# Optimization experiments

Hardware: AMD Instinct MI355X
Metric: run time of the kernel (lower is better)

## Reference

```python
import jax, jax.numpy as jnp
import numpy as np

N, F, D = 50000, 64, 3
E = 800000
H = 128          # local MLP hidden / output dim
G = 256          # global MLP output dim


def _init_linear(key, fan_in, fan_out):
    kw, kb = jax.random.split(key)
    W = jax.random.normal(kw, (fan_in, fan_out), dtype=jnp.float32) / np.sqrt(fan_in)
    b = jax.random.normal(kb, (fan_out,), dtype=jnp.float32) * 0.01
    return W, b


def setup_inputs() -> dict:
    key = jax.random.key(0)
    kx, kp, ke, k1, k2, kg = jax.random.split(key, 6)
    x = jax.random.normal(kx, (N, F), dtype=jnp.float32)
    pos = jax.random.uniform(kp, (N, D), dtype=jnp.float32)
    edge_index = jax.random.randint(ke, (2, E), 0, N, dtype=jnp.int64)
    W1, b1 = _init_linear(k1, F + D, H)   # local_nn layer 1
    W2, b2 = _init_linear(k2, H, H)       # local_nn layer 2
    Wg, bg = _init_linear(kg, H, G)       # global_nn
    return {"x": x, "pos": pos, "W1": W1, "b1": b1, "W2": W2, "b2": b2,
            "Wg": Wg, "bg": bg, "edge_index": edge_index}


def reference(x, pos, W1, b1, W2, b2, Wg, bg, edge_index):
    n = x.shape[0]
    # add self loops (duplicate edges are harmless under max-reduction)
    loops = jnp.arange(n, dtype=edge_index.dtype)
    ei = jnp.concatenate([edge_index, jnp.stack([loops, loops])], axis=1)
    row, col = ei[0], ei[1]            # row = target i, col = neighbor j
    rel = pos[col] - pos[row]          # [E+N, D]
    h = jnp.concatenate([x[col], rel], axis=1)          # [E+N, F+D]
    h = jax.nn.relu(h @ W1 + b1)                         # local MLP
    h = jax.nn.relu(h @ W2 + b2)                         # [E+N, H]
    agg = jax.ops.segment_max(h, row, num_segments=n)    # scatter-max per node
    out = jax.nn.relu(agg @ Wg + bg)                      # global MLP [N, G]
    return out
```

## Files before the change

### kernel.cpp

```cpp
#include <hip/hip_runtime.h>

typedef __attribute__((ext_vector_type(4))) float f32x4;
typedef __attribute__((ext_vector_type(8))) short bf16x8;

#define EDGE_GRID 2048
#define OUT_GRID  512

__device__ __forceinline__ unsigned int f2bf(float f) {
    unsigned int u = __float_as_uint(f);
    return (u + 0x7FFFu + ((u >> 16) & 1u)) >> 16;
}

__global__ __launch_bounds__(256) void u_kernel(
    const float* __restrict__ x, const float* __restrict__ W1,
    const float* __restrict__ b1, unsigned short* __restrict__ u, int N)
{
    __shared__ float sx[8][64];
    const int t = threadIdx.x;
    const int base = blockIdx.x * 8;
    for (int i = t; i < 512; i += 256) {
        const int node = base + (i >> 6);
        sx[i >> 6][i & 63] = (node < N) ? x[(size_t)node * 64 + (i & 63)] : 0.0f;
    }
    __syncthreads();
    const int half = t >> 7, col = t & 127;
    const float bias = b1[col];
    float acc[4] = {bias, bias, bias, bias};
#pragma unroll 8
    for (int k = 0; k < 64; ++k) {
        const float w = W1[k * 128 + col];
#pragma unroll
        for (int j = 0; j < 4; ++j)
            acc[j] = fmaf(sx[half * 4 + j][k], w, acc[j]);
    }
#pragma unroll
    for (int j = 0; j < 4; ++j) {
        const int node = base + half * 4 + j;
        if (node < N) u[(size_t)node * 128 + col] = (unsigned short)f2bf(acc[j]);
    }
}

__global__ void prep_kernel(const float* __restrict__ W2, const float* __restrict__ Wg,
                            unsigned short* __restrict__ W2t, unsigned short* __restrict__ Wgt)
{
    const int i = blockIdx.x * 256 + threadIdx.x;
    if (i < 16384) {
        const int n = i >> 7, k = i & 127;
        W2t[i] = (unsigned short)f2bf(W2[k * 128 + n]);
    } else if (i < 49152) {
        const int j = i - 16384;
        const int n = j >> 7, k = j & 127;
        Wgt[j] = (unsigned short)f2bf(Wg[k * 256 + n]);
    }
}

__global__ void count_kernel(const int* __restrict__ ei, int* __restrict__ deg,
                             int E, int nTot)
{
    const int i = blockIdx.x * 256 + threadIdx.x;
    if (i < nTot) {
        const int row = (i < E) ? ei[i] : i - E;
        atomicAdd(deg + row, 1);
    }
}

__global__ __launch_bounds__(256) void scan1_kernel(
    const int* __restrict__ deg, int* __restrict__ offs, int* __restrict__ bsums, int N)
{
    __shared__ int sc[256];
    const int t = threadIdx.x;
    const int i0 = blockIdx.x * 1024 + t * 4;
    int v0 = (i0 + 0 < N) ? deg[i0 + 0] : 0;
    int v1 = (i0 + 1 < N) ? deg[i0 + 1] : 0;
    int v2 = (i0 + 2 < N) ? deg[i0 + 2] : 0;
    int v3 = (i0 + 3 < N) ? deg[i0 + 3] : 0;
    const int s = v0 + v1 + v2 + v3;
    sc[t] = s;
    __syncthreads();
    for (int off = 1; off < 256; off <<= 1) {
        const int val = (t >= off) ? sc[t - off] : 0;
        __syncthreads();
        sc[t] += val;
        __syncthreads();
    }
    int run = sc[t] - s;
    if (i0 + 0 < N) offs[i0 + 0] = run; run += v0;
    if (i0 + 1 < N) offs[i0 + 1] = run; run += v1;
    if (i0 + 2 < N) offs[i0 + 2] = run; run += v2;
    if (i0 + 3 < N) offs[i0 + 3] = run;
    if (t == 255) bsums[blockIdx.x] = sc[255];
}

__global__ void scan2_kernel(int* __restrict__ bsums, int NB)
{
    __shared__ int sc[64];
    const int t = threadIdx.x;
    const int v = (t < NB) ? bsums[t] : 0;
    sc[t] = v;
    __syncthreads();
    for (int off = 1; off < 64; off <<= 1) {
        const int val = (t >= off) ? sc[t - off] : 0;
        __syncthreads();
        sc[t] += val;
        __syncthreads();
    }
    if (t < NB) bsums[t] = sc[t] - v;
}

__global__ void scan3_kernel(int* __restrict__ offs, const int* __restrict__ bsums, int N)
{
    const int i = blockIdx.x * 256 + threadIdx.x;
    if (i < N) offs[i] += bsums[i >> 10];
}

__global__ void scatter_kernel(const int* __restrict__ ei, const int* __restrict__ offs,
                               int* __restrict__ cursor, int* __restrict__ srow,
                               int* __restrict__ scol, int E, int nTot)
{
    const int i = blockIdx.x * 256 + threadIdx.x;
    if (i < nTot) {
        int row, col;
        if (i < E) { row = ei[i]; col = ei[E + i]; }
        else       { row = col = i - E; }
        const int p = atomicAdd(cursor + row, 1);
        const int q = offs[row] + p;
        srow[q] = row;
        scol[q] = col;
    }
}

__global__ __launch_bounds__(256, 4) void edge_kernel(
    const unsigned short* __restrict__ u, const float* __restrict__ pos,
    const float* __restrict__ W1, const float* __restrict__ b2,
    const unsigned short* __restrict__ W2t, const int* __restrict__ srow,
    const int* __restrict__ scol, unsigned int* __restrict__ agg,
    int nTot, int nTiles)
{
    __shared__ unsigned short sh1[2][4096];
    __shared__ float          sh2[4096];
    __shared__ float          sW1p[384];
    __shared__ int            sRowL[2][32];

    const int t = threadIdx.x;
    const int wv = t >> 6, lane = t & 63;
    const int m = lane & 15, g = lane >> 4;
    const int n0 = wv * 32 + m;
    const int e_h1 = t >> 3, kc = (t & 7) * 16;
    const int cR = t & 127, hR = t >> 7;

    bf16x8 bfr[2][4];
#pragma unroll
    for (int nb = 0; nb < 2; ++nb)
#pragma unroll
        for (int ks = 0; ks < 4; ++ks)
            bfr[nb][ks] = *(const bf16x8*)(W2t + (size_t)(n0 + nb * 16) * 128 + (ks * 4 + g) * 8);
    const float bia0 = b2[n0], bia1 = b2[n0 + 16];

    for (int i = t; i < 384; i += 256) sW1p[i] = W1[64 * 128 + i];
    __syncthreads();

    auto gather = [&](int tile, int& c, float& r0, float& r1, float& r2,
                      uint4& ua, uint4& ub, int& rowStage) {
        c = -1; rowStage = -1;
        if (tile < nTiles) {
            const int p = tile * 32 + e_h1;
            if (p < nTot) {
                c = scol[p];
                const int r = srow[p];
                r0 = pos[c * 3 + 0] - pos[r * 3 + 0];
                r1 = pos[c * 3 + 1] - pos[r * 3 + 1];
                r2 = pos[c * 3 + 2] - pos[r * 3 + 2];
                const uint4* up = (const uint4*)(u + (size_t)c * 128 + kc);
                ua = up[0]; ub = up[1];
            }
            if (t < 32) {
                const int p2 = tile * 32 + t;
                rowStage = (p2 < nTot) ? srow[p2] : -1;
            }
        }
    };
    auto computeH1 = [&](int buf, int c, float r0, float r1, float r2,
                         uint4 ua, uint4 ub, int rowStage) {
        unsigned int ow[8] = {0,0,0,0,0,0,0,0};
        if (c >= 0) {
            const unsigned int uw[8] = {ua.x, ua.y, ua.z, ua.w, ub.x, ub.y, ub.z, ub.w};
#pragma unroll
            for (int j = 0; j < 8; ++j) {
                const int k = kc + j * 2;
                float lo = __uint_as_float(uw[j] << 16);
                float hi = __uint_as_float(uw[j] & 0xFFFF0000u);
                lo = fmaf(r0, sW1p[k],     fmaf(r1, sW1p[128 + k],     fmaf(r2, sW1p[256 + k],     lo)));
                hi = fmaf(r0, sW1p[k + 1], fmaf(r1, sW1p[128 + k + 1], fmaf(r2, sW1p[256 + k + 1], hi)));
                ow[j] = f2bf(fmaxf(lo, 0.0f)) | (f2bf(fmaxf(hi, 0.0f)) << 16);
            }
        }
        const int g0 = e_h1 * 16 + (t & 7) * 2;
        ((int4*)sh1[buf])[(g0)     ^ (e_h1 & 7)] = make_int4(ow[0], ow[1], ow[2], ow[3]);
        ((int4*)sh1[buf])[(g0 + 1) ^ (e_h1 & 7)] = make_int4(ow[4], ow[5], ow[6], ow[7]);
        if (t < 32) sRowL[buf][t] = rowStage;
    };

    {
        int c, rs; float r0 = 0, r1 = 0, r2 = 0; uint4 ua = {0,0,0,0}, ub = {0,0,0,0};
        gather(blockIdx.x, c, r0, r1, r2, ua, ub, rs);
        computeH1(0, c, r0, r1, r2, ua, ub, rs);
    }
    __syncthreads();

    int b = 0;
    for (int tile = blockIdx.x; tile < nTiles; tile += EDGE_GRID, b ^= 1) {
        const int nextTile = tile + EDGE_GRID;

        int c, rs; float r0 = 0, r1 = 0, r2 = 0; uint4 ua = {0,0,0,0}, ub = {0,0,0,0};
        gather(nextTile, c, r0, r1, r2, ua, ub, rs);

        {
            f32x4 acc0 = {0,0,0,0}, acc1 = {0,0,0,0}, acc2 = {0,0,0,0}, acc3 = {0,0,0,0};
            const unsigned short* s1 = sh1[b];
#pragma unroll
            for (int ks = 0; ks < 4; ++ks) {
                const int slot = ks * 4 + g;
                const bf16x8 a0 = *(const bf16x8*)&s1[(m        * 16 + (slot ^ (m & 7))) << 3];
                const bf16x8 a1 = *(const bf16x8*)&s1[((m + 16) * 16 + (slot ^ (m & 7))) << 3];
                acc0 = __builtin_amdgcn_mfma_f32_16x16x32_bf16(a0, bfr[0][ks], acc0, 0, 0, 0);
                acc1 = __builtin_amdgcn_mfma_f32_16x16x32_bf16(a0, bfr[1][ks], acc1, 0, 0, 0);
                acc2 = __builtin_amdgcn_mfma_f32_16x16x32_bf16(a1, bfr[0][ks], acc2, 0, 0, 0);
                acc3 = __builtin_amdgcn_mfma_f32_16x16x32_bf16(a1, bfr[1][ks], acc3, 0, 0, 0);
            }
#pragma unroll
            for (int rg = 0; rg < 4; ++rg) {
                const int e0 = g * 4 + rg, e1 = 16 + g * 4 + rg;
                sh2[e0 * 128 + ((n0      + e0 * 4) & 127)] = fmaxf(acc0[rg] + bia0, 0.0f);
                sh2[e0 * 128 + ((n0 + 16 + e0 * 4) & 127)] = fmaxf(acc1[rg] + bia1, 0.0f);
                sh2[e1 * 128 + ((n0      + e1 * 4) & 127)] = fmaxf(acc2[rg] + bia0, 0.0f);
                sh2[e1 * 128 + ((n0 + 16 + e1 * 4) & 127)] = fmaxf(acc3[rg] + bia1, 0.0f);
            }
        }
        __syncthreads();

        {
            float run = 0.0f; int cur = -1;
            const int ebase = hR * 16;
            for (int i = 0; i < 16; ++i) {
                const int e = ebase + i;
                const int r = sRowL[b][e];
                if (r < 0) break;
                const float v = sh2[e * 128 + ((cR + e * 4) & 127)];
                if (r != cur) {
                    if (cur >= 0) {
                        const unsigned int bits = __float_as_uint(run);
                        unsigned int* dst = agg + (size_t)cur * 128 + cR;
                        if (bits > *dst) atomicMax(dst, bits);
                    }
                    cur = r; run = v;
                } else run = fmaxf(run, v);
            }
            if (cur >= 0) {
                const unsigned int bits = __float_as_uint(run);
                unsigned int* dst = agg + (size_t)cur * 128 + cR;
                if (bits > *dst) atomicMax(dst, bits);
            }
        }

        if (nextTile < nTiles)
            computeH1(b ^ 1, c, r0, r1, r2, ua, ub, rs);
        __syncthreads();
    }
}

__global__ __launch_bounds__(256, 2) void out_kernel(
    const float* __restrict__ agg, const unsigned short* __restrict__ Wgt,
    const float* __restrict__ bg, float* __restrict__ out, int N, int nTiles)
{
    extern __shared__ char smem[];
    unsigned short* sWgt = (unsigned short*)smem;
    unsigned short* sA   = (unsigned short*)(smem + 65536);
    float*          sbg  = (float*)(smem + 73728);

    const int t = threadIdx.x;
    for (int i = t; i < 4096; i += 256) {
        const int n = i >> 4;
        ((int4*)sWgt)[i ^ (n & 7)] = ((const int4*)Wgt)[i];
    }
    if (t < 256) sbg[t] = bg[t];
    __syncthreads();

    const int wv = t >> 6, lane = t & 63;
    const int m = lane & 15, g = lane >> 4;
    const int eA = t >> 3, kcA = (t & 7) * 16;

    for (int tile = blockIdx.x; tile < nTiles; tile += OUT_GRID) {
        const int tbase = tile * 32;

        {
            unsigned int ow[8] = {0,0,0,0,0,0,0,0};
            const int node = tbase + eA;
            if (node < N) {
                const float4* ap = (const float4*)(agg + (size_t)node * 128 + kcA);
#pragma unroll
                for (int j = 0; j < 4; ++j) {
                    const float4 v = ap[j];
                    ow[j * 2 + 0] = f2bf(v.x) | (f2bf(v.y) << 16);
                    ow[j * 2 + 1] = f2bf(v.z) | (f2bf(v.w) << 16);
                }
            }
            const int g0 = eA * 16 + (t & 7) * 2;
            ((int4*)sA)[(g0)     ^ (eA & 7)] = make_int4(ow[0], ow[1], ow[2], ow[3]);
            ((int4*)sA)[(g0 + 1) ^ (eA & 7)] = make_int4(ow[4], ow[5], ow[6], ow[7]);
        }
        __syncthreads();

        f32x4 acc[2][4] = {{{0,0,0,0},{0,0,0,0},{0,0,0,0},{0,0,0,0}},
                           {{0,0,0,0},{0,0,0,0},{0,0,0,0},{0,0,0,0}}};
#pragma unroll
        for (int ks = 0; ks < 4; ++ks) {
            const int slot = ks * 4 + g;
            const bf16x8 a0 = *(const bf16x8*)&sA[(m        * 16 + (slot ^ (m & 7))) << 3];
            const bf16x8 a1 = *(const bf16x8*)&sA[((m + 16) * 16 + (slot ^ (m & 7))) << 3];
#pragma unroll
            for (int nt = 0; nt < 4; ++nt) {
                const int n = wv * 64 + nt * 16 + m;
                const bf16x8 bfrag = *(const bf16x8*)&sWgt[(n * 16 + (slot ^ (m & 7))) << 3];
                acc[0][nt] = __builtin_amdgcn_mfma_f32_16x16x32_bf16(a0, bfrag, acc[0][nt], 0, 0, 0);
                acc[1][nt] = __builtin_amdgcn_mfma_f32_16x16x32_bf16(a1, bfrag, acc[1][nt], 0, 0, 0);
            }
        }
#pragma unroll
        for (int mg = 0; mg < 2; ++mg)
#pragma unroll
        for (int nt = 0; nt < 4; ++nt) {
            const int n = wv * 64 + nt * 16 + m;
            const float bias = sbg[n];
#pragma unroll
            for (int rg = 0; rg < 4; ++rg) {
                const int node = tbase + mg * 16 + g * 4 + rg;
                if (node < N)
                    out[(size_t)node * 256 + n] = fmaxf(acc[mg][nt][rg] + bias, 0.0f);
            }
        }
        __syncthreads();
    }
}

extern "C" void kernel_launch(void* const* d_in, const int* in_sizes, int n_in,
                              void* d_out, int out_size, void* d_ws, size_t ws_size,
                              hipStream_t stream)
{
    const float* x   = (const float*)d_in[0];
    const float* pos = (const float*)d_in[1];
    const float* W1  = (const float*)d_in[2];
    const float* b1  = (const float*)d_in[3];
    const float* W2  = (const float*)d_in[4];
    const float* b2  = (const float*)d_in[5];
    const float* Wg  = (const float*)d_in[6];
    const float* bg  = (const float*)d_in[7];
    const int*   ei  = (const int*)d_in[8];
    float* out = (float*)d_out;

    const int N    = in_sizes[1] / 3;
    const int E    = in_sizes[8] / 2;
    const int nTot = E + N;

    size_t off = 0;
    auto alloc = [&](size_t bytes) -> void* {
        void* p = (char*)d_ws + off;
        off += (bytes + 255) & ~(size_t)255;
        return p;
    };
    unsigned short* u      = (unsigned short*)alloc((size_t)N * 128 * 2);
    unsigned int*   agg    = (unsigned int*)  alloc((size_t)N * 128 * 4);
    int*            deg    = (int*)           alloc((size_t)N * 4);
    int*            offs   = (int*)           alloc((size_t)N * 4);
    int*            cursor = (int*)           alloc((size_t)N * 4);
    int*            srow   = (int*)           alloc((size_t)nTot * 4);
    int*            scol   = (int*)           alloc((size_t)nTot * 4);
    unsigned short* W2t    = (unsigned short*)alloc(16384 * 2);
    unsigned short* Wgt    = (unsigned short*)alloc(32768 * 2);
    int*            bsums  = (int*)           alloc(64 * 4);

    hipMemsetAsync(agg,    0, (size_t)N * 128 * 4, stream);
    hipMemsetAsync(deg,    0, (size_t)N * 4,       stream);
    hipMemsetAsync(cursor, 0, (size_t)N * 4,       stream);

    hipLaunchKernelGGL(prep_kernel, dim3(192), dim3(256), 0, stream, W2, Wg, W2t, Wgt);
    hipLaunchKernelGGL(u_kernel, dim3((N + 7) / 8), dim3(256), 0, stream, x, W1, b1, u, N);
    hipLaunchKernelGGL(count_kernel, dim3((nTot + 255) / 256), dim3(256), 0, stream,
                       ei, deg, E, nTot);
    const int NB = (N + 1023) / 1024;
    hipLaunchKernelGGL(scan1_kernel, dim3(NB), dim3(256), 0, stream, deg, offs, bsums, N);
    hipLaunchKernelGGL(scan2_kernel, dim3(1), dim3(64), 0, stream, bsums, NB);
    hipLaunchKernelGGL(scan3_kernel, dim3((N + 255) / 256), dim3(256), 0, stream,
                       offs, bsums, N);
    hipLaunchKernelGGL(scatter_kernel, dim3((nTot + 255) / 256), dim3(256), 0, stream,
                       ei, offs, cursor, srow, scol, E, nTot);

    const int nTilesE = (nTot + 31) / 32;
    hipLaunchKernelGGL(edge_kernel, dim3(EDGE_GRID), dim3(256), 0, stream,
                       u, pos, W1, b2, W2t, srow, scol, agg, nTot, nTilesE);

    const int nTilesO = (N + 31) / 32;
    const int out_shmem = 65536 + 8192 + 1024;
    hipFuncSetAttribute((const void*)out_kernel,
                        hipFuncAttributeMaxDynamicSharedMemorySize, out_shmem);
    hipLaunchKernelGGL(out_kernel, dim3(OUT_GRID), dim3(256), out_shmem, stream,
                       (const float*)agg, Wgt, bg, out, N, nTilesO);
}
```

Measured before the change: 378.5 us.

## Fuse prep kernels, single-block scan, register-resident weights, retuned edge pipeline

Merges the u, count and weight-transpose kernels into one launch and replaces the three-kernel scan with a single 1024-thread block scan. The scatter reuses the degree counter through atomicSub, so the cursor buffer and its memset go away. In the edge kernel the h1 buffer becomes single, W1 rows are padded in shared memory to avoid bank conflicts, the next tile's h1 is written before the scatter-max, and occupancy is raised. The output kernel keeps Wg fragments in registers instead of a 64KB shared copy, allowing more blocks and a larger grid. The single-block scan serializes the prefix sum, and the heavier register use may cause spills.

```diff
diff --git a/kernel.cpp b/kernel.cpp
--- a/kernel.cpp
+++ b/kernel.cpp
@@ -1,120 +1,122 @@
 #include <hip/hip_runtime.h>
+#include <hip/hip_bf16.h>
 
 typedef __attribute__((ext_vector_type(4))) float f32x4;
 typedef __attribute__((ext_vector_type(8))) short bf16x8;
 
-#define EDGE_GRID 2048
-#define OUT_GRID  512
-
-__device__ __forceinline__ unsigned int f2bf(float f) {
-    unsigned int u = __float_as_uint(f);
-    return (u + 0x7FFFu + ((u >> 16) & 1u)) >> 16;
-}
-
-__global__ __launch_bounds__(256) void u_kernel(
+#define EDGE_GRID 1536
+#define OUT_GRID  1024
+
+__device__ __forceinline__ unsigned int packbf(float lo, float hi) {
+    __hip_bfloat16 l = __float2bfloat16(lo), h = __float2bfloat16(hi);
+    const unsigned short lu = *reinterpret_cast<unsigned short*>(&l);
+    const unsigned short hu = *reinterpret_cast<unsigned short*>(&h);
+    return (unsigned int)lu | ((unsigned int)hu << 16);
+}
+__device__ __forceinline__ unsigned short bf1(float f) {
+    __hip_bfloat16 v = __float2bfloat16(f);
+    return *reinterpret_cast<unsigned short*>(&v);
+}
+
+__global__ __launch_bounds__(256) void prep_kernel(
     const float* __restrict__ x, const float* __restrict__ W1,
-    const float* __restrict__ b1, unsigned short* __restrict__ u, int N)
+    const float* __restrict__ b1, const float* __restrict__ W2,
+    const float* __restrict__ Wg, const int* __restrict__ ei,
+    unsigned short* __restrict__ u, unsigned short* __restrict__ W2t,
+    unsigned short* __restrict__ Wgt, int* __restrict__ deg,
+    int N, int E, int nTot, int NB_U, int NB_C)
 {
     __shared__ float sx[8][64];
+    const int blk = blockIdx.x;
     const int t = threadIdx.x;
-    const int base = blockIdx.x * 8;
-    for (int i = t; i < 512; i += 256) {
-        const int node = base + (i >> 6);
-        sx[i >> 6][i & 63] = (node < N) ? x[(size_t)node * 64 + (i & 63)] : 0.0f;
-    }
-    __syncthreads();
-    const int half = t >> 7, col = t & 127;
-    const float bias = b1[col];
-    float acc[4] = {bias, bias, bias, bias};
+    if (blk < NB_U) {
+        const int base = blk * 8;
+        for (int i = t; i < 512; i += 256) {
+            const int node = base + (i >> 6);
+            sx[i >> 6][i & 63] = (node < N) ? x[(size_t)node * 64 + (i & 63)] : 0.0f;
+        }
+        __syncthreads();
+        const int half = t >> 7, col = t & 127;
+        const float bias = b1[col];
+        float acc[4] = {bias, bias, bias, bias};
 #pragma unroll 8
-    for (int k = 0; k < 64; ++k) {
-        const float w = W1[k * 128 + col];
-#pragma unroll
-        for (int j = 0; j < 4; ++j)
-            acc[j] = fmaf(sx[half * 4 + j][k], w, acc[j]);
-    }
-#pragma unroll
-    for (int j = 0; j < 4; ++j) {
-        const int node = base + half * 4 + j;
-        if (node < N) u[(size_t)node * 128 + col] = (unsigned short)f2bf(acc[j]);
-    }
-}
-
-__global__ void prep_kernel(const float* __restrict__ W2, const float* __restrict__ Wg,
-                            unsigned short* __restrict__ W2t, unsigned short* __restrict__ Wgt)
-{
-    const int i = blockIdx.x * 256 + threadIdx.x;
-    if (i < 16384) {
-        const int n = i >> 7, k = i & 127;
-        W2t[i] = (unsigned short)f2bf(W2[k * 128 + n]);
-    } else if (i < 49152) {
-        const int j = i - 16384;
-        const int n = j >> 7, k = j & 127;
-        Wgt[j] = (unsigned short)f2bf(Wg[k * 256 + n]);
-    }
-}
-
-__global__ void count_kernel(const int* __restrict__ ei, int* __restrict__ deg,
-                             int E, int nTot)
-{
-    const int i = blockIdx.x * 256 + threadIdx.x;
-    if (i < nTot) {
-        const int row = (i < E) ? ei[i] : i - E;
-        atomicAdd(deg + row, 1);
-    }
-}
-
-__global__ __launch_bounds__(256) void scan1_kernel(
-    const int* __restrict__ deg, int* __restrict__ offs, int* __restrict__ bsums, int N)
-{
-    __shared__ int sc[256];
+        for (int k = 0; k < 64; ++k) {
+            const float w = W1[k * 128 + col];
+#pragma unroll
+            for (int j = 0; j < 4; ++j)
+                acc[j] = fmaf(sx[half * 4 + j][k], w, acc[j]);
+        }
+#pragma unroll
+        for (int j = 0; j < 4; ++j) {
+            const int node = base + half * 4 + j;
+            if (node < N) u[(size_t)node * 128 + col] = bf1(acc[j]);
+        }
+    } else if (blk < NB_U + NB_C) {
+        const int i = (blk - NB_U) * 256 + t;
+        if (i < nTot) {
+            const int row = (i < E) ? ei[i] : i - E;
+            atomicAdd(deg + row, 1);
+        }
+    } else {
+        const int i = (blk - NB_U - NB_C) * 256 + t;
+        if (i < 16384) {
+            const int n = i >> 7, k = i & 127;
+            W2t[i] = bf1(W2[k * 128 + n]);
+        } else if (i < 49152) {
+            const int j = i - 16384;
+            const int n = j >> 7, k = j & 127;
+            Wgt[j] = bf1(Wg[k * 256 + n]);
+        }
+    }
+}
+
+__global__ __launch_bounds__(1024) void scan_kernel(
+    const int* __restrict__ deg, int* __restrict__ offs, int N)
+{
+    __shared__ int sc[1024];
     const int t = threadIdx.x;
-    const int i0 = blockIdx.x * 1024 + t * 4;
-    int v0 = (i0 + 0 < N) ? deg[i0 + 0] : 0;
-    int v1 = (i0 + 1 < N) ? deg[i0 + 1] : 0;
-    int v2 = (i0 + 2 < N) ? deg[i0 + 2] : 0;
-    int v3 = (i0 + 3 < N) ? deg[i0 + 3] : 0;
-    const int s = v0 + v1 + v2 + v3;
+    const int c0 = t * 52;
+    int v[52];
+    int s = 0;
+#pragma unroll
+    for (int j4 = 0; j4 < 13; ++j4) {
+        const int idx = c0 + j4 * 4;
+        int4 d = {0, 0, 0, 0};
+        if (idx + 3 < N) d = *(const int4*)(deg + idx);
+        else {
+            if (idx     < N) d.x = deg[idx];
+            if (idx + 1 < N) d.y = deg[idx + 1];
+            if (idx + 2 < N) d.z = deg[idx + 2];
+        }
+        v[j4*4+0] = s; s += d.x;
+        v[j4*4+1] = s; s += d.y;
+        v[j4*4+2] = s; s += d.z;
+        v[j4*4+3] = s; s += d.w;
+    }
     sc[t] = s;
     __syncthreads();
-    for (int off = 1; off < 256; off <<= 1) {
+    for (int off = 1; off < 1024; off <<= 1) {
         const int val = (t >= off) ? sc[t - off] : 0;
         __syncthreads();
         sc[t] += val;
         __syncthreads();
     }
-    int run = sc[t] - s;
-    if (i0 + 0 < N) offs[i0 + 0] = run; run += v0;
-    if (i0 + 1 < N) offs[i0 + 1] = run; run += v1;
-    if (i0 + 2 < N) offs[i0 + 2] = run; run += v2;
-    if (i0 + 3 < N) offs[i0 + 3] = run;
-    if (t == 255) bsums[blockIdx.x] = sc[255];
-}
-
-__global__ void scan2_kernel(int* __restrict__ bsums, int NB)
-{
-    __shared__ int sc[64];
-    const int t = threadIdx.x;
-    const int v = (t < NB) ? bsums[t] : 0;
-    sc[t] = v;
-    __syncthreads();
-    for (int off = 1; off < 64; off <<= 1) {
-        const int val = (t >= off) ? sc[t - off] : 0;
-        __syncthreads();
-        sc[t] += val;
-        __syncthreads();
-    }
-    if (t < NB) bsums[t] = sc[t] - v;
-}
-
-__global__ void scan3_kernel(int* __restrict__ offs, const int* __restrict__ bsums, int N)
-{
-    const int i = blockIdx.x * 256 + threadIdx.x;
-    if (i < N) offs[i] += bsums[i >> 10];
+    const int base = sc[t] - s;
+#pragma unroll
+    for (int j4 = 0; j4 < 13; ++j4) {
+        const int idx = c0 + j4 * 4;
+        const int4 o = {base + v[j4*4], base + v[j4*4+1], base + v[j4*4+2], base + v[j4*4+3]};
+        if (idx + 3 < N) *(int4*)(offs + idx) = o;
+        else {
+            if (idx     < N) offs[idx]     = o.x;
+            if (idx + 1 < N) offs[idx + 1] = o.y;
+            if (idx + 2 < N) offs[idx + 2] = o.z;
+        }
+    }
 }
 
 __global__ void scatter_kernel(const int* __restrict__ ei, const int* __restrict__ offs,
-                               int* __restrict__ cursor, int* __restrict__ srow,
+                               int* __restrict__ deg, int* __restrict__ srow,
                                int* __restrict__ scol, int E, int nTot)
 {
     const int i = blockIdx.x * 256 + threadIdx.x;
@@ -122,30 +124,31 @@
         int row, col;
         if (i < E) { row = ei[i]; col = ei[E + i]; }
         else       { row = col = i - E; }
-        const int p = atomicAdd(cursor + row, 1);
+        const int p = atomicSub(deg + row, 1) - 1;
         const int q = offs[row] + p;
         srow[q] = row;
         scol[q] = col;
     }
 }
 
-__global__ __launch_bounds__(256, 4) void edge_kernel(
+__global__ __launch_bounds__(256, 6) void edge_kernel(
     const unsigned short* __restrict__ u, const float* __restrict__ pos,
     const float* __restrict__ W1, const float* __restrict__ b2,
     const unsigned short* __restrict__ W2t, const int* __restrict__ srow,
     const int* __restrict__ scol, unsigned int* __restrict__ agg,
     int nTot, int nTiles)
 {
-    __shared__ unsigned short sh1[2][4096];
+    __shared__ unsigned short sh1[4096];
     __shared__ float          sh2[4096];
-    __shared__ float          sW1p[384];
+    __shared__ float          sW1p[480];
     __shared__ int            sRowL[2][32];
 
     const int t = threadIdx.x;
     const int wv = t >> 6, lane = t & 63;
     const int m = lane & 15, g = lane >> 4;
     const int n0 = wv * 32 + m;
-    const int e_h1 = t >> 3, kc = (t & 7) * 16;
+    const int e_h1 = t >> 3, s8 = t & 7, kc = s8 * 16;
+    const int wb = s8 * 18;
     const int cR = t & 127, hR = t >> 7;
 
     bf16x8 bfr[2][4];
@@ -156,7 +159,10 @@
             bfr[nb][ks] = *(const bf16x8*)(W2t + (size_t)(n0 + nb * 16) * 128 + (ks * 4 + g) * 8);
     const float bia0 = b2[n0], bia1 = b2[n0 + 16];
 
-    for (int i = t; i < 384; i += 256) sW1p[i] = W1[64 * 128 + i];
+    for (int i = t; i < 384; i += 256) {
+        const int r = i >> 7, k = i & 127;
+        sW1p[r * 160 + k + 2 * (k >> 4)] = W1[64 * 128 + i];
+    }
     __syncthreads();
 
     auto gather = [&](int tile, int& c, float& r0, float& r1, float& r2,
@@ -186,17 +192,17 @@
             const unsigned int uw[8] = {ua.x, ua.y, ua.z, ua.w, ub.x, ub.y, ub.z, ub.w};
 #pragma unroll
             for (int j = 0; j < 8; ++j) {
-                const int k = kc + j * 2;
+                const int wk = wb + 2 * j;
                 float lo = __uint_as_float(uw[j] << 16);
                 float hi = __uint_as_float(uw[j] & 0xFFFF0000u);
-                lo = fmaf(r0, sW1p[k],     fmaf(r1, sW1p[128 + k],     fmaf(r2, sW1p[256 + k],     lo)));
-                hi = fmaf(r0, sW1p[k + 1], fmaf(r1, sW1p[128 + k + 1], fmaf(r2, sW1p[256 + k + 1], hi)));
-                ow[j] = f2bf(fmaxf(lo, 0.0f)) | (f2bf(fmaxf(hi, 0.0f)) << 16);
-            }
-        }
-        const int g0 = e_h1 * 16 + (t & 7) * 2;
-        ((int4*)sh1[buf])[(g0)     ^ (e_h1 & 7)] = make_int4(ow[0], ow[1], ow[2], ow[3]);
-        ((int4*)sh1[buf])[(g0 + 1) ^ (e_h1 & 7)] = make_int4(ow[4], ow[5], ow[6], ow[7]);
+                lo = fmaf(r0, sW1p[wk],       fmaf(r1, sW1p[160 + wk],     fmaf(r2, sW1p[320 + wk],     lo)));
+                hi = fmaf(r0, sW1p[wk + 1],   fmaf(r1, sW1p[160 + wk + 1], fmaf(r2, sW1p[320 + wk + 1], hi)));
+                ow[j] = packbf(fmaxf(lo, 0.0f), fmaxf(hi, 0.0f));
+            }
+        }
+        const int g0 = e_h1 * 16 + s8 * 2;
+        ((int4*)sh1)[(g0)     ^ (e_h1 & 7)] = make_int4(ow[0], ow[1], ow[2], ow[3]);
+        ((int4*)sh1)[(g0 + 1) ^ (e_h1 & 7)] = make_int4(ow[4], ow[5], ow[6], ow[7]);
         if (t < 32) sRowL[buf][t] = rowStage;
     };
 
@@ -216,12 +222,11 @@
 
         {
             f32x4 acc0 = {0,0,0,0}, acc1 = {0,0,0,0}, acc2 = {0,0,0,0}, acc3 = {0,0,0,0};
-            const unsigned short* s1 = sh1[b];
 #pragma unroll
             for (int ks = 0; ks < 4; ++ks) {
                 const int slot = ks * 4 + g;
-                const bf16x8 a0 = *(const bf16x8*)&s1[(m        * 16 + (slot ^ (m & 7))) << 3];
-                const bf16x8 a1 = *(const bf16x8*)&s1[((m + 16) * 16 + (slot ^ (m & 7))) << 3];
+                const bf16x8 a0 = *(const bf16x8*)&sh1[(m        * 16 + (slot ^ (m & 7))) << 3];
+                const bf16x8 a1 = *(const bf16x8*)&sh1[((m + 16) * 16 + (slot ^ (m & 7))) << 3];
                 acc0 = __builtin_amdgcn_mfma_f32_16x16x32_bf16(a0, bfr[0][ks], acc0, 0, 0, 0);
                 acc1 = __builtin_amdgcn_mfma_f32_16x16x32_bf16(a0, bfr[1][ks], acc1, 0, 0, 0);
                 acc2 = __builtin_amdgcn_mfma_f32_16x16x32_bf16(a1, bfr[0][ks], acc2, 0, 0, 0);
@@ -237,6 +242,9 @@
             }
         }
         __syncthreads();
+
+        if (nextTile < nTiles)
+            computeH1(b ^ 1, c, r0, r1, r2, ua, ub, rs);
 
         {
             float run = 0.0f; int cur = -1;
@@ -261,33 +269,31 @@
                 if (bits > *dst) atomicMax(dst, bits);
             }
         }
-
-        if (nextTile < nTiles)
-            computeH1(b ^ 1, c, r0, r1, r2, ua, ub, rs);
-        __syncthreads();
-    }
-}
-
-__global__ __launch_bounds__(256, 2) void out_kernel(
+        __syncthreads();
+    }
+}
+
+__global__ __launch_bounds__(256, 4) void out_kernel(
     const float* __restrict__ agg, const unsigned short* __restrict__ Wgt,
     const float* __restrict__ bg, float* __restrict__ out, int N, int nTiles)
 {
-    extern __shared__ char smem[];
-    unsigned short* sWgt = (unsigned short*)smem;
-    unsigned short* sA   = (unsigned short*)(smem + 65536);
-    float*          sbg  = (float*)(smem + 73728);
+    __shared__ unsigned short sA[4096];
 
     const int t = threadIdx.x;
-    for (int i = t; i < 4096; i += 256) {
-        const int n = i >> 4;
-        ((int4*)sWgt)[i ^ (n & 7)] = ((const int4*)Wgt)[i];
-    }
-    if (t < 256) sbg[t] = bg[t];
-    __syncthreads();
-
     const int wv = t >> 6, lane = t & 63;
     const int m = lane & 15, g = lane >> 4;
     const int eA = t >> 3, kcA = (t & 7) * 16;
+
+    bf16x8 wfr[4][4];
+    float bgv[4];
+#pragma unroll
+    for (int nt = 0; nt < 4; ++nt) {
+        const int n = wv * 64 + nt * 16 + m;
+#pragma unroll
+        for (int ks = 0; ks < 4; ++ks)
+            wfr[nt][ks] = *(const bf16x8*)(Wgt + (size_t)n * 128 + (ks * 4 + g) * 8);
+        bgv[nt] = bg[n];
+    }
 
     for (int tile = blockIdx.x; tile < nTiles; tile += OUT_GRID) {
         const int tbase = tile * 32;
@@ -300,8 +306,8 @@
 #pragma unroll
                 for (int j = 0; j < 4; ++j) {
                     const float4 v = ap[j];
-                    ow[j * 2 + 0] = f2bf(v.x) | (f2bf(v.y) << 16);
-                    ow[j * 2 + 1] = f2bf(v.z) | (f2bf(v.w) << 16);
+                    ow[j * 2 + 0] = packbf(v.x, v.y);
+                    ow[j * 2 + 1] = packbf(v.z, v.w);
                 }
             }
             const int g0 = eA * 16 + (t & 7) * 2;
@@ -319,10 +325,8 @@
             const bf16x8 a1 = *(const bf16x8*)&sA[((m + 16) * 16 + (slot ^ (m & 7))) << 3];
 #pragma unroll
             for (int nt = 0; nt < 4; ++nt) {
-                const int n = wv * 64 + nt * 16 + m;
-                const bf16x8 bfrag = *(const bf16x8*)&sWgt[(n * 16 + (slot ^ (m & 7))) << 3];
-                acc[0][nt] = __builtin_amdgcn_mfma_f32_16x16x32_bf16(a0, bfrag, acc[0][nt], 0, 0, 0);
-                acc[1][nt] = __builtin_amdgcn_mfma_f32_16x16x32_bf16(a1, bfrag, acc[1][nt], 0, 0, 0);
+                acc[0][nt] = __builtin_amdgcn_mfma_f32_16x16x32_bf16(a0, wfr[nt][ks], acc[0][nt], 0, 0, 0);
+                acc[1][nt] = __builtin_amdgcn_mfma_f32_16x16x32_bf16(a1, wfr[nt][ks], acc[1][nt], 0, 0, 0);
             }
         }
 #pragma unroll
@@ -330,12 +334,11 @@
 #pragma unroll
         for (int nt = 0; nt < 4; ++nt) {
             const int n = wv * 64 + nt * 16 + m;
-            const float bias = sbg[n];
 #pragma unroll
             for (int rg = 0; rg < 4; ++rg) {
                 const int node = tbase + mg * 16 + g * 4 + rg;
                 if (node < N)
-                    out[(size_t)node * 256 + n] = fmaxf(acc[mg][nt][rg] + bias, 0.0f);
+                    out[(size_t)node * 256 + n] = fmaxf(acc[mg][nt][rg] + bgv[nt], 0.0f);
             }
         }
         __syncthreads();
@@ -367,41 +370,34 @@
         off += (bytes + 255) & ~(size_t)255;
         return p;
     };
-    unsigned short* u      = (unsigned short*)alloc((size_t)N * 128 * 2);
-    unsigned int*   agg    = (unsigned int*)  alloc((size_t)N * 128 * 4);
-    int*            deg    = (int*)           alloc((size_t)N * 4);
-    int*            offs   = (int*)           alloc((size_t)N * 4);
-    int*            cursor = (int*)           alloc((size_t)N * 4);
-    int*            srow   = (int*)           alloc((size_t)nTot * 4);
-    int*            scol   = (int*)           alloc((size_t)nTot * 4);
-    unsigned short* W2t    = (unsigned short*)alloc(16384 * 2);
-    unsigned short* Wgt    = (unsigned short*)alloc(32768 * 2);
-    int*            bsums  = (int*)           alloc(64 * 4);
-
-    hipMemsetAsync(agg,    0, (size_t)N * 128 * 4, stream);
-    hipMemsetAsync(deg,    0, (size_t)N * 4,       stream);
-    hipMemsetAsync(cursor, 0, (size_t)N * 4,       stream);
-
-    hipLaunchKernelGGL(prep_kernel, dim3(192), dim3(256), 0, stream, W2, Wg, W2t, Wgt);
-    hipLaunchKernelGGL(u_kernel, dim3((N + 7) / 8), dim3(256), 0, stream, x, W1, b1, u, N);
-    hipLaunchKernelGGL(count_kernel, dim3((nTot + 255) / 256), dim3(256), 0, stream,
-                       ei, deg, E, nTot);
-    const int NB = (N + 1023) / 1024;
-    hipLaunchKernelGGL(scan1_kernel, dim3(NB), dim3(256), 0, stream, deg, offs, bsums, N);
-    hipLaunchKernelGGL(scan2_kernel, dim3(1), dim3(64), 0, stream, bsums, NB);
-    hipLaunchKernelGGL(scan3_kernel, dim3((N + 255) / 256), dim3(256), 0, stream,
-                       offs, bsums, N);
+    unsigned short* u    = (unsigned short*)alloc((size_t)N * 128 * 2);
+    unsigned int*   agg  = (unsigned int*)  alloc((size_t)N * 128 * 4);
+    int*            deg  = (int*)           alloc((size_t)N * 4);
+    int*            offs = (int*)           alloc((size_t)N * 4);
+    int*            srow = (int*)           alloc((size_t)nTot * 4);
+    int*            scol = (int*)           alloc((size_t)nTot * 4);
+    unsigned short* W2t  = (unsigned short*)alloc(16384 * 2);
+    unsigned short* Wgt  = (unsigned short*)alloc(32768 * 2);
+
+    hipMemsetAsync(agg, 0, (size_t)N * 128 * 4, stream);
+    hipMemsetAsync(deg, 0, (size_t)N * 4, stream);
+
+    const int NB_U = (N + 7) / 8;
+    const int NB_C = (nTot + 255) / 256;
+    const int NB_T = 192;
+    hipLaunchKernelGGL(prep_kernel, dim3(NB_U + NB_C + NB_T), dim3(256), 0, stream,
+                       x, W1, b1, W2, Wg, ei, u, W2t, Wgt, deg, N, E, nTot, NB_U, NB_C);
+
+    hipLaunchKernelGGL(scan_kernel, dim3(1), dim3(1024), 0, stream, deg, offs, N);
+
     hipLaunchKernelGGL(scatter_kernel, dim3((nTot + 255) / 256), dim3(256), 0, stream,
-                       ei, offs, cursor, srow, scol, E, nTot);
+                       ei, offs, deg, srow, scol, E, nTot);
 
     const int nTilesE = (nTot + 31) / 32;
     hipLaunchKernelGGL(edge_kernel, dim3(EDGE_GRID), dim3(256), 0, stream,
                        u, pos, W1, b2, W2t, srow, scol, agg, nTot, nTilesE);
 
     const int nTilesO = (N + 31) / 32;
-    const int out_shmem = 65536 + 8192 + 1024;
-    hipFuncSetAttribute((const void*)out_kernel,
-                        hipFuncAttributeMaxDynamicSharedMemorySize, out_shmem);
-    hipLaunchKernelGGL(out_kernel, dim3(OUT_GRID), dim3(256), out_shmem, stream,
+    hipLaunchKernelGGL(out_kernel, dim3(OUT_GRID), dim3(256), 0, stream,
                        (const float*)agg, Wgt, bg, out, N, nTilesO);
 }
```

After: 442.0 us. +16.8%, slower.
